# Optimization experiments

Hardware: AMD Instinct MI355X
Metric: run time of the kernel (lower is better)

The kernel has to match this reference:

```python
import jax, jax.numpy as jnp
import numpy as np

N, T, D, H1, H2, NH = 4096, 2048, 256, 128, 32, 4
ALPHA = 0.2  # LeakyReLU slope in GAT
NEG = -9e15  # mask value for non-edges


def _gat(x, adj, W, a_src, a_dst, fc_W, fc_b):
    # Multi-head GAT (pygat style), heads stacked on leading axis, then Linear fc.
    Wh = jnp.einsum('nd,hde->hne', x, W)                    # [NH, n, d_out]
    f = jnp.einsum('hne,he->hn', Wh, a_src)                 # a^T [Wh_i || .]
    g = jnp.einsum('hne,he->hn', Wh, a_dst)                 # a^T [. || Wh_j]
    e = jax.nn.leaky_relu(f[:, :, None] + g[:, None, :], ALPHA)  # [NH, n, n]
    e = jnp.where(adj[None, :, :] > 0, e, NEG)
    att = jax.nn.softmax(e, axis=-1)
    h = jax.nn.elu(jnp.einsum('hnm,hme->hne', att, Wh))     # concat=True -> ELU
    h = jnp.transpose(h, (1, 0, 2)).reshape(x.shape[0], -1)  # [n, NH*d_out]
    return h @ fc_W + fc_b


def setup_inputs() -> dict:
    key = jax.random.key(0)
    ks = jax.random.split(key, 24)
    s = 0.1
    x = jax.random.normal(ks[0], (N, D), jnp.float32)
    t_x = jax.random.normal(ks[1], (T, D), jnp.float32)
    adj = (jax.random.uniform(ks[2], (N, N)) < 0.005).astype(jnp.float32) + jnp.eye(N, dtype=jnp.float32)
    t_adj = (jax.random.uniform(ks[3], (T, T)) < 0.01).astype(jnp.float32) + jnp.eye(T, dtype=jnp.float32)
    tfidf_x = jax.random.uniform(ks[4], (T, N), jnp.float32) * 0.01
    p = lambda k, shp: jax.random.normal(k, shp, jnp.float32) * s
    return {
        'x': x, 'adj': adj, 't_x': t_x, 't_adj': t_adj, 'tfidf_x': tfidf_x,
        # concept-graph MHGAT (in D -> per-head D, concat NH*D -> fc -> D)
        'gat_W': p(ks[5], (NH, D, D)), 'gat_asrc': p(ks[6], (NH, D)), 'gat_adst': p(ks[7], (NH, D)),
        'gat_fcW': p(ks[8], (NH * D, D)), 'gat_fcb': jnp.zeros((D,), jnp.float32),
        # text-graph MHGAT
        't_W': p(ks[9], (NH, D, D)), 't_asrc': p(ks[10], (NH, D)), 't_adst': p(ks[11], (NH, D)),
        't_fcW': p(ks[12], (NH * D, D)), 't_fcb': jnp.zeros((D,), jnp.float32),
        # gated fusion fc
        'fus_W': p(ks[13], (D, D)), 'fus_b': jnp.zeros((D,), jnp.float32),
        # GCN encoder weights (Kipf VGAE GraphConvolution: adj @ (x @ W))
        'gc1_W': p(ks[14], (D, H1)), 'gc2_W': p(ks[15], (H1, H2)), 'gc3_W': p(ks[16], (H1, H2)),
    }


def reference(x, adj, t_x, t_adj, tfidf_x,
              gat_W, gat_asrc, gat_adst, gat_fcW, gat_fcb,
              t_W, t_asrc, t_adst, t_fcW, t_fcb,
              fus_W, fus_b, gc1_W, gc2_W, gc3_W):
    # gated fusion of concept-graph and text-graph GAT outputs (eval mode, dropout off)
    concept = _gat(x, adj, gat_W, gat_asrc, gat_adst, gat_fcW, gat_fcb)      # [N, D]
    gat_text = _gat(t_x, t_adj, t_W, t_asrc, t_adst, t_fcW, t_fcb)           # [T, D]
    c_text = tfidf_x.T @ gat_text                                            # [N, D]
    z = jax.nn.sigmoid(concept + c_text)
    fusion = (z * concept + (1.0 - z) * c_text) @ fus_W + fus_b              # [N, D]
    # GCN VAE encoder
    h1 = jax.nn.relu(adj @ (fusion @ gc1_W))                                 # [N, H1]
    mu = adj @ (h1 @ gc2_W)                                                  # [N, H2]
    logvar = adj @ (h1 @ gc3_W)                                              # [N, H2]
    # eval-mode reparameterize -> z_lat = mu; decoder act is identity in GCNModelVAE
    recon = mu @ mu.T                                                        # [N, N]
    return recon, mu, logvar
```

## Files before the change

### kernel.cpp

```cpp
#include <hip/hip_runtime.h>
#include <hip/hip_bf16.h>

#define MAX_E 128
typedef __attribute__((ext_vector_type(8))) short bf16x8;
typedef __attribute__((ext_vector_type(4))) float f32x4;

__device__ __forceinline__ unsigned short f2bf(float f) {
    union { float f; unsigned u; } a; a.f = f;
    unsigned r = a.u + 0x7FFFu + ((a.u >> 16) & 1u);
    return (unsigned short)(r >> 16);
}
__device__ __forceinline__ float bf2f(unsigned short s) {
    union { unsigned u; float f; } a; a.u = ((unsigned)s) << 16; return a.f;
}
__device__ __forceinline__ float wave_sum(float v) {
#pragma unroll
    for (int o = 1; o < 64; o <<= 1) v += __shfl_xor(v, o, 64);
    return v;
}
__device__ __forceinline__ float wave_max(float v) {
#pragma unroll
    for (int o = 1; o < 64; o <<= 1) v = fmaxf(v, __shfl_xor(v, o, 64));
    return v;
}

#define MAXJ 16
struct TJobs {
    const float* src[MAXJ];
    unsigned short* dst[MAXJ];
    int R[MAXJ], C[MAXJ], tb[MAXJ];
    int njobs;
};

__global__ __launch_bounds__(256) void prep_k(
        const float* __restrict__ adj, const float* __restrict__ t_adj,
        int* __restrict__ cnt, int* __restrict__ eidx_c, int* __restrict__ eidx_t,
        const float* __restrict__ gat_W, const float* __restrict__ gat_asrc,
        const float* __restrict__ gat_adst, const float* __restrict__ t_W,
        const float* __restrict__ t_asrc, const float* __restrict__ t_adst,
        float* __restrict__ APDP,
        const float* __restrict__ fus_W, const float* __restrict__ fus_b,
        const float* __restrict__ gc1_W, unsigned short* __restrict__ W2T,
        float* __restrict__ B2, int w2_base, TJobs tj) {
    __shared__ float smem[2080];
    int bid = blockIdx.x, tid = threadIdx.x;
    if (bid < 6144) {
        int* s_cnt = (int*)smem;
        if (tid == 0) *s_cnt = 0;
        __syncthreads();
        if (bid < 4096) {
            const float4* ar = (const float4*)(adj + (size_t)bid * 4096);
            int* er = eidx_c + (size_t)bid * MAX_E;
            float4 v0 = ar[tid], v1 = ar[tid + 256], v2 = ar[tid + 512], v3 = ar[tid + 768];
            float va[16] = {v0.x, v0.y, v0.z, v0.w, v1.x, v1.y, v1.z, v1.w,
                            v2.x, v2.y, v2.z, v2.w, v3.x, v3.y, v3.z, v3.w};
#pragma unroll
            for (int it = 0; it < 4; it++) {
                int jb = (tid + it * 256) * 4;
#pragma unroll
                for (int c = 0; c < 4; c++) {
                    float vv = va[it * 4 + c];
                    if (vv > 0.f) {
                        int p = atomicAdd(s_cnt, 1);
                        if (p < MAX_E) er[p] = (jb + c) | (vv > 1.5f ? 0x40000000 : 0);
                    }
                }
            }
        } else {
            int r = bid - 4096;
            const float4* ar = (const float4*)(t_adj + (size_t)r * 2048);
            int* er = eidx_t + (size_t)r * MAX_E;
            float4 v0 = ar[tid], v1 = ar[tid + 256];
            float va[8] = {v0.x, v0.y, v0.z, v0.w, v1.x, v1.y, v1.z, v1.w};
#pragma unroll
            for (int it = 0; it < 2; it++) {
                int jb = (tid + it * 256) * 4;
#pragma unroll
                for (int c = 0; c < 4; c++) {
                    if (va[it * 4 + c] > 0.f) {
                        int p = atomicAdd(s_cnt, 1);
                        if (p < MAX_E) er[p] = jb + c;
                    }
                }
            }
        }
        __syncthreads();
        if (tid == 0) cnt[bid] = *s_cnt < MAX_E ? *s_cnt : MAX_E;
    } else if (bid < 6152) {
        int pb = bid - 6144, h = pb & 3, g = pb >> 2, d = tid;
        const float* W  = g ? t_W : gat_W;
        const float* as = g ? t_asrc : gat_asrc;
        const float* ad = g ? t_adst : gat_adst;
        float* sa = smem; float* sd = smem + 256;
        sa[d] = as[h * 256 + d]; sd[d] = ad[h * 256 + d];
        __syncthreads();
        const float* wr = W + (size_t)h * 65536 + (size_t)d * 256;
        float ap = 0.f, dp = 0.f;
        for (int e = 0; e < 256; e++) { float w = wr[e]; ap += w * sa[e]; dp += w * sd[e]; }
        APDP[g * 1024 + h * 256 + d] = ap;
        APDP[2048 + g * 1024 + h * 256 + d] = dp;
    } else if (bid < w2_base) {
        int local = bid - 6152;
        int j = 0;
        while (j + 1 < tj.njobs && local >= tj.tb[j + 1]) j++;
        local -= tj.tb[j];
        int R = tj.R[j], C = tj.C[j];
        int xt = C >> 5;
        int tx = local % xt, ty = local / xt;
        const float* in = tj.src[j];
        unsigned short* outp = tj.dst[j];
        float (*t)[33] = (float(*)[33])smem;
        int jj = tid & 31, ii = tid >> 5;
        int r0 = ty * 32, c0 = tx * 32;
#pragma unroll
        for (int k = 0; k < 4; k++) { int rl = ii + k * 8; t[rl][jj] = in[(size_t)(r0 + rl) * C + c0 + jj]; }
        __syncthreads();
#pragma unroll
        for (int k = 0; k < 4; k++) { int cl = ii + k * 8; outp[(size_t)(c0 + cl) * R + r0 + jj] = f2bf(t[jj][cl]); }
    } else if (bid < w2_base + 32) {
        int bW = bid - w2_base;
        int n0 = (bW & 3) * 32, k0 = (bW >> 2) * 32;
        int nn = tid & 31, kb = (tid >> 5) * 4;
        float (*s_a)[65] = (float(*)[65])smem;
        float acc[4] = {0.f, 0.f, 0.f, 0.f};
        for (int ec = 0; ec < 4; ec++) {
            for (int t = tid; t < 32 * 64; t += 256) {
                int kk2 = t >> 6, ee = t & 63;
                s_a[kk2][ee] = fus_W[(size_t)(k0 + kk2) * 256 + ec * 64 + ee];
            }
            __syncthreads();
            for (int ee = 0; ee < 64; ee++) {
                float b = gc1_W[(size_t)(ec * 64 + ee) * 128 + n0 + nn];
#pragma unroll
                for (int c = 0; c < 4; c++) acc[c] += s_a[kb + c][ee] * b;
            }
            __syncthreads();
        }
#pragma unroll
        for (int c = 0; c < 4; c++)
            W2T[(size_t)(n0 + nn) * 256 + k0 + kb + c] = f2bf(acc[c]);
    } else {
        if (tid < 128) {
            float acc = 0.f;
            for (int k = 0; k < 256; k++) acc += fus_b[k] * gc1_W[(size_t)k * 128 + tid];
            B2[tid] = acc;
        }
    }
}

__global__ __launch_bounds__(256) void whfg_k(
        const float* __restrict__ x, const float* __restrict__ t_x,
        const unsigned short* __restrict__ WT, const unsigned short* __restrict__ TWT,
        unsigned short* __restrict__ WHC, unsigned short* __restrict__ WHT,
        const float* __restrict__ APDP, float* __restrict__ FC, float* __restrict__ GC,
        float* __restrict__ FT, float* __restrict__ GT) {
    __shared__ __align__(16) unsigned short As[64 * 40], Bs[64 * 40];
    int bid = blockIdx.x, tid = threadIdx.x;
    if (bid < 1536) {
        int g, xk, y, h;
        if (bid < 1024) { g = 0; xk = bid & 3; y = (bid >> 2) & 63; h = bid >> 8; }
        else { int b2 = bid - 1024; g = 1; xk = b2 & 3; y = (b2 >> 2) & 31; h = b2 >> 7; }
        const float* Af = g ? t_x : x;
        const unsigned short* Bt = (g ? TWT : WT) + h * 65536;
        unsigned short* C = (g ? WHT : WHC) + h * 256;
        int m0 = y * 64, n0 = xk * 64;
        int wave = tid >> 6, lane = tid & 63, quad = lane >> 4, r = lane & 15;
        int lrow = tid >> 2, lcol8 = (tid & 3) * 8;
        f32x4 acc[4] = {{0.f,0.f,0.f,0.f},{0.f,0.f,0.f,0.f},{0.f,0.f,0.f,0.f},{0.f,0.f,0.f,0.f}};
        for (int k0 = 0; k0 < 256; k0 += 32) {
            const float* ap = Af + (size_t)(m0 + lrow) * 256 + k0 + lcol8;
            float4 a0 = *(const float4*)ap;
            float4 a1 = *(const float4*)(ap + 4);
            ushort4 u0 = {f2bf(a0.x), f2bf(a0.y), f2bf(a0.z), f2bf(a0.w)};
            ushort4 u1 = {f2bf(a1.x), f2bf(a1.y), f2bf(a1.z), f2bf(a1.w)};
            uint4 bv = *(const uint4*)(Bt + (size_t)(n0 + lrow) * 256 + k0 + lcol8);
            *(ushort4*)(&As[lrow * 40 + lcol8]) = u0;
            *(ushort4*)(&As[lrow * 40 + lcol8 + 4]) = u1;
            *(uint4*)(&Bs[lrow * 40 + lcol8]) = bv;
            __syncthreads();
            bf16x8 af = *(const bf16x8*)(&As[(wave * 16 + r) * 40 + quad * 8]);
#pragma unroll
            for (int nj = 0; nj < 4; nj++) {
                bf16x8 bfr = *(const bf16x8*)(&Bs[(nj * 16 + r) * 40 + quad * 8]);
                acc[nj] = __builtin_amdgcn_mfma_f32_16x16x32_bf16(af, bfr, acc[nj], 0, 0, 0);
            }
            __syncthreads();
        }
#pragma unroll
        for (int nj = 0; nj < 4; nj++) {
            int n = n0 + nj * 16 + r;
#pragma unroll
            for (int reg = 0; reg < 4; reg++) {
                int m = m0 + wave * 16 + quad * 4 + reg;
                C[(size_t)m * 1024 + n] = f2bf(acc[nj][reg]);
            }
        }
    } else {
        int b = bid - 1536;
        int h = tid >> 6, lane = tid & 63;
        const float* xr; float* F; float* G; const float* AP; const float* DP; int n, i;
        if (b < 4096) { i = b; xr = x + (size_t)i * 256; F = FC; G = GC; AP = APDP; DP = APDP + 2048; n = 4096; }
        else { i = b - 4096; xr = t_x + (size_t)i * 256; F = FT; G = GT; AP = APDP + 1024; DP = APDP + 3072; n = 2048; }
        float vf = 0.f, vg = 0.f;
#pragma unroll
        for (int c = 0; c < 4; c++) {
            int d = c * 64 + lane;
            float xv = xr[d];
            vf += xv * AP[h * 256 + d];
            vg += xv * DP[h * 256 + d];
        }
        vf = wave_sum(vf); vg = wave_sum(vg);
        if (lane == 0) { F[h * n + i] = vf; G[h * n + i] = vg; }
    }
}

__global__ __launch_bounds__(256) void agg_all_k(const unsigned short* __restrict__ WHC,
        const unsigned short* __restrict__ WHT, const float* __restrict__ FC,
        const float* __restrict__ GC, const float* __restrict__ FT,
        const float* __restrict__ GT, const int* __restrict__ cnt,
        const int* __restrict__ eidx_c, const int* __restrict__ eidx_t,
        unsigned short* __restrict__ HCC, unsigned short* __restrict__ HCT) {
    int b = blockIdx.x, tid = threadIdx.x;
    int h = tid >> 6, lane = tid & 63;
    int ne = cnt[b];
    const unsigned short* WH; const float* F; const float* G; const int* ei;
    unsigned short* HC; int n, i;
    if (b < 4096) { i = b; n = 4096; WH = WHC; F = FC; G = GC; ei = eidx_c + (size_t)i * MAX_E; HC = HCC; }
    else { i = b - 4096; n = 2048; WH = WHT; F = FT; G = GT; ei = eidx_t + (size_t)i * MAX_E; HC = HCT; }
    __shared__ int s_col[MAX_E];
    __shared__ float s_w[4][MAX_E];
    for (int e = tid; e < ne; e += 256) s_col[e] = ei[e] & 0xFFFF;
    __syncthreads();
    float fi = F[h * n + i];
    float lmax = -1e30f;
    for (int e = lane; e < ne; e += 64) {
        float xv = fi + G[h * n + s_col[e]];
        xv = xv >= 0.f ? xv : 0.2f * xv;
        s_w[h][e] = xv;
        lmax = fmaxf(lmax, xv);
    }
    lmax = wave_max(lmax);
    float lsum = 0.f;
    for (int e = lane; e < ne; e += 64) {
        float w = __expf(s_w[h][e] - lmax);
        s_w[h][e] = w;
        lsum += w;
    }
    lsum = wave_sum(lsum);
    float inv = 1.f / lsum;
    float a0 = 0.f, a1 = 0.f, a2 = 0.f, a3 = 0.f;
    const unsigned short* base = WH + h * 256 + lane * 4;
    for (int e = 0; e < ne; e++) {
        float w = s_w[h][e];
        ushort4 q = *(const ushort4*)(base + (size_t)s_col[e] * 1024);
        a0 += w * bf2f(q.x); a1 += w * bf2f(q.y); a2 += w * bf2f(q.z); a3 += w * bf2f(q.w);
    }
    a0 *= inv; a1 *= inv; a2 *= inv; a3 *= inv;
    a0 = a0 > 0.f ? a0 : __expf(a0) - 1.f;
    a1 = a1 > 0.f ? a1 : __expf(a1) - 1.f;
    a2 = a2 > 0.f ? a2 : __expf(a2) - 1.f;
    a3 = a3 > 0.f ? a3 : __expf(a3) - 1.f;
    ushort4 st; st.x = f2bf(a0); st.y = f2bf(a1); st.z = f2bf(a2); st.w = f2bf(a3);
    *(ushort4*)(HC + (size_t)i * 1024 + h * 256 + lane * 4) = st;
}

__device__ __forceinline__ void mfma_core(const unsigned short* __restrict__ A,
        const unsigned short* __restrict__ Bt, int K, int m0, int n0,
        unsigned short* As, unsigned short* Bs, f32x4 acc[4]) {
    int tid = threadIdx.x;
    int wave = tid >> 6, lane = tid & 63, quad = lane >> 4, r = lane & 15;
    int lrow = tid >> 2, lcol8 = (tid & 3) * 8;
    for (int k0 = 0; k0 < K; k0 += 32) {
        uint4 av = *(const uint4*)(A + (size_t)(m0 + lrow) * K + k0 + lcol8);
        uint4 bv = *(const uint4*)(Bt + (size_t)(n0 + lrow) * K + k0 + lcol8);
        *(uint4*)(&As[lrow * 40 + lcol8]) = av;
        *(uint4*)(&Bs[lrow * 40 + lcol8]) = bv;
        __syncthreads();
        bf16x8 af = *(const bf16x8*)(&As[(wave * 16 + r) * 40 + quad * 8]);
#pragma unroll
        for (int nj = 0; nj < 4; nj++) {
            bf16x8 bfr = *(const bf16x8*)(&Bs[(nj * 16 + r) * 40 + quad * 8]);
            acc[nj] = __builtin_amdgcn_mfma_f32_16x16x32_bf16(af, bfr, acc[nj], 0, 0, 0);
        }
        __syncthreads();
    }
}

__global__ __launch_bounds__(256) void fc_both_k(const unsigned short* __restrict__ HCC,
        const unsigned short* __restrict__ HCT, const unsigned short* __restrict__ FCWT,
        const unsigned short* __restrict__ TFCWT, const float* __restrict__ fcb,
        const float* __restrict__ tfcb, float* __restrict__ CPT,
        unsigned short* __restrict__ GTT) {
    __shared__ __align__(16) unsigned short As[64 * 40], Bs[64 * 40];
    int z = blockIdx.z;
    int M = z ? 2048 : 4096;
    int m0 = blockIdx.y * 64, n0 = blockIdx.x * 64;
    if (m0 >= M) return;
    const unsigned short* A = z ? HCT : HCC;
    const unsigned short* Bt = z ? TFCWT : FCWT;
    const float* bias = z ? tfcb : fcb;
    f32x4 acc[4] = {{0.f,0.f,0.f,0.f},{0.f,0.f,0.f,0.f},{0.f,0.f,0.f,0.f},{0.f,0.f,0.f,0.f}};
    mfma_core(A, Bt, 1024, m0, n0, As, Bs, acc);
    int tid = threadIdx.x, wave = tid >> 6, lane = tid & 63, quad = lane >> 4, r = lane & 15;
#pragma unroll
    for (int nj = 0; nj < 4; nj++) {
        int n = n0 + nj * 16 + r;
        float bv = bias[n];
        if (z == 0) {
#pragma unroll
            for (int reg = 0; reg < 4; reg++) {
                int m = m0 + wave * 16 + quad * 4 + reg;
                CPT[(size_t)m * 256 + n] = acc[nj][reg] + bv;
            }
        } else {
            int mb = m0 + wave * 16 + quad * 4;
            ushort4 st;
            st.x = f2bf(acc[nj][0] + bv); st.y = f2bf(acc[nj][1] + bv);
            st.z = f2bf(acc[nj][2] + bv); st.w = f2bf(acc[nj][3] + bv);
            *(ushort4*)(GTT + (size_t)n * 2048 + mb) = st;
        }
    }
}

__global__ __launch_bounds__(256) void ctext_gate_k(
        const float* __restrict__ tfidf, const unsigned short* __restrict__ GTT,
        const float* __restrict__ CPT, unsigned short* __restrict__ FUSEIN) {
    __shared__ __align__(16) unsigned short As[64 * 40], Bs[64 * 40];
    int tid = threadIdx.x;
    int wave = tid >> 6, lane = tid & 63, quad = lane >> 4, r = lane & 15;
    int m0 = blockIdx.y * 64, n0 = blockIdx.x * 64;
    int kk = tid >> 3;
    int jj = tid & 7;
    int b  = kk >> 3, t7 = kk & 7;
    int lrow = tid >> 2, lcol8 = (tid & 3) * 8;
    int mfr = wave * 16 + r;
    int cswz = (mfr >> 3) & 3;
    f32x4 acc[4] = {{0.f,0.f,0.f,0.f},{0.f,0.f,0.f,0.f},{0.f,0.f,0.f,0.f},{0.f,0.f,0.f,0.f}};
    for (int k0 = 0; k0 < 2048; k0 += 32) {
        const float* ap = tfidf + (size_t)(k0 + kk) * 4096 + m0 + jj * 8;
        float4 a0 = *(const float4*)ap;
        float4 a1 = *(const float4*)(ap + 4);
        uint4 bv = *(const uint4*)(GTT + (size_t)(n0 + lrow) * 2048 + k0 + lcol8);
        float av[8] = {a0.x, a0.y, a0.z, a0.w, a1.x, a1.y, a1.z, a1.w};
#pragma unroll
        for (int i = 0; i < 8; i++) {
            int m = jj * 8 + i;
            As[m * 40 + ((b ^ (jj & 3)) * 8) + t7] = f2bf(av[i]);
        }
        *(uint4*)(&Bs[lrow * 40 + lcol8]) = bv;
        __syncthreads();
        bf16x8 af = *(const bf16x8*)(&As[mfr * 40 + ((quad ^ cswz) * 8)]);
#pragma unroll
        for (int nj = 0; nj < 4; nj++) {
            bf16x8 bfr = *(const bf16x8*)(&Bs[(nj * 16 + r) * 40 + quad * 8]);
            acc[nj] = __builtin_amdgcn_mfma_f32_16x16x32_bf16(af, bfr, acc[nj], 0, 0, 0);
        }
        __syncthreads();
    }
#pragma unroll
    for (int nj = 0; nj < 4; nj++) {
        int n = n0 + nj * 16 + r;
#pragma unroll
        for (int reg = 0; reg < 4; reg++) {
            int m = m0 + wave * 16 + quad * 4 + reg;
            float v = acc[nj][reg];
            float c = CPT[(size_t)m * 256 + n];
            float z = 1.f / (1.f + __expf(-(c + v)));
            FUSEIN[(size_t)m * 256 + n] = f2bf(z * c + (1.f - z) * v);
        }
    }
}

template <int EP>
__global__ __launch_bounds__(256) void gemm_ep_k(const unsigned short* __restrict__ A,
        const unsigned short* __restrict__ Bt, const float* __restrict__ bias,
        void* __restrict__ Cv, int M, int N, int K, int ldc) {
    __shared__ __align__(16) unsigned short As[64 * 40], Bs[64 * 40];
    int m0 = blockIdx.y * 64, n0 = blockIdx.x * 64;
    if (m0 >= M) return;
    f32x4 acc[4] = {{0.f,0.f,0.f,0.f},{0.f,0.f,0.f,0.f},{0.f,0.f,0.f,0.f},{0.f,0.f,0.f,0.f}};
    mfma_core(A, Bt, K, m0, n0, As, Bs, acc);
    int tid = threadIdx.x, wave = tid >> 6, lane = tid & 63, quad = lane >> 4, r = lane & 15;
#pragma unroll
    for (int nj = 0; nj < 4; nj++) {
        int n = n0 + nj * 16 + r;
        float bv = (EP == 1) ? bias[n] : 0.f;
#pragma unroll
        for (int reg = 0; reg < 4; reg++) {
            int m = m0 + wave * 16 + quad * 4 + reg;
            ((float*)Cv)[(size_t)m * ldc + n] = acc[nj][reg] + bv;
        }
    }
}

__global__ void spmm_h1_k(const int* __restrict__ cnt, const int* __restrict__ eidx,
                          const float* __restrict__ T1, unsigned short* __restrict__ H1B) {
    int i = blockIdx.x, tid = threadIdx.x;
    int ne = cnt[i];
    __shared__ int s_e[MAX_E];
    for (int e = tid; e < ne; e += 128) s_e[e] = eidx[(size_t)i * MAX_E + e];
    __syncthreads();
    float acc = 0.f;
    for (int e = 0; e < ne; e++) {
        int p = s_e[e];
        float v = (p & 0x40000000) ? 2.f : 1.f;
        acc += v * T1[(size_t)(p & 0xFFFF) * 128 + tid];
    }
    H1B[(size_t)i * 128 + tid] = f2bf(fmaxf(acc, 0.f));
}

__global__ void spmm_mu_k(const int* __restrict__ cnt, const int* __restrict__ eidx,
                          const unsigned short* __restrict__ H1B,
                          const unsigned short* __restrict__ GC23WT,
                          float* __restrict__ MU, float* __restrict__ LOGVAR,
                          unsigned short* __restrict__ MUBF) {
    int i = blockIdx.x, tid = threadIdx.x;
    int ne = cnt[i];
    __shared__ int s_e[MAX_E];
    __shared__ float s_a2[128];
    for (int e = tid; e < ne; e += 128) s_e[e] = eidx[(size_t)i * MAX_E + e];
    __syncthreads();
    float acc = 0.f;
    for (int e = 0; e < ne; e++) {
        int p = s_e[e];
        float v = (p & 0x40000000) ? 2.f : 1.f;
        acc += v * bf2f(H1B[(size_t)(p & 0xFFFF) * 128 + tid]);
    }
    s_a2[tid] = acc;
    __syncthreads();
    if (tid < 64) {
        const unsigned short* w = GC23WT + tid * 128;
        float o = 0.f;
        for (int k = 0; k < 128; k++) o += s_a2[k] * bf2f(w[k]);
        if (tid < 32) { MU[(size_t)i * 32 + tid] = o; MUBF[(size_t)i * 32 + tid] = f2bf(o); }
        else LOGVAR[(size_t)i * 32 + (tid - 32)] = o;
    }
}

extern "C" void kernel_launch(void* const* d_in, const int* in_sizes, int n_in,
                              void* d_out, int out_size, void* d_ws, size_t ws_size,
                              hipStream_t stream) {
    const float* x        = (const float*)d_in[0];
    const float* adj      = (const float*)d_in[1];
    const float* t_x      = (const float*)d_in[2];
    const float* t_adj    = (const float*)d_in[3];
    const float* tfidf    = (const float*)d_in[4];
    const float* gat_W    = (const float*)d_in[5];
    const float* gat_asrc = (const float*)d_in[6];
    const float* gat_adst = (const float*)d_in[7];
    const float* gat_fcW  = (const float*)d_in[8];
    const float* gat_fcb  = (const float*)d_in[9];
    const float* t_W      = (const float*)d_in[10];
    const float* t_asrc   = (const float*)d_in[11];
    const float* t_adst   = (const float*)d_in[12];
    const float* t_fcW    = (const float*)d_in[13];
    const float* t_fcb    = (const float*)d_in[14];
    const float* fus_W    = (const float*)d_in[15];
    const float* fus_b    = (const float*)d_in[16];
    const float* gc1_W    = (const float*)d_in[17];
    const float* gc2_W    = (const float*)d_in[18];
    const float* gc3_W    = (const float*)d_in[19];

    float* out = (float*)d_out;
    float* ws  = (float*)d_ws;

    unsigned short* WHC   = (unsigned short*)(ws + 0);
    unsigned short* HCC   = (unsigned short*)(ws + 2097152);
    unsigned short* WHT   = (unsigned short*)(ws + 4194304);
    unsigned short* HCT   = (unsigned short*)(ws + 5242880);
    float* CPT            = ws + 6291456;
    unsigned short* GTT   = (unsigned short*)(ws + 7340032);
    unsigned short* FUSEIN= (unsigned short*)(ws + 7602176);
    float* T1             = ws + 8126464;
    unsigned short* H1B   = (unsigned short*)(ws + 8650752);
    unsigned short* MUBF  = (unsigned short*)(ws + 8912896);
    float* FC             = ws + 8978432;
    float* GC             = ws + 8994816;
    float* FT             = ws + 9011200;
    float* GT             = ws + 9019392;
    float* APDP           = ws + 9027584;
    unsigned short* WT    = (unsigned short*)(ws + 9031680);
    unsigned short* TWT   = (unsigned short*)(ws + 9162752);
    unsigned short* FCWT  = (unsigned short*)(ws + 9293824);
    unsigned short* TFCWT = (unsigned short*)(ws + 9424896);
    unsigned short* W2T   = (unsigned short*)(ws + 9555968);
    float* B2             = ws + 9572352;
    unsigned short* GC23WT= (unsigned short*)(ws + 9572480);
    int* ECNT             = (int*)(ws + 9576576);
    int* EIDX_C           = (int*)(ws + 9582720);
    int* EIDX_T           = (int*)(ws + 10107008);
    float* MU     = out + (size_t)4096 * 4096;
    float* LOGVAR = MU + (size_t)4096 * 32;

    TJobs tj = {};
    int nj = 0, tb = 0;
    auto add = [&](const float* s, unsigned short* d, int R, int C) {
        tj.src[nj] = s; tj.dst[nj] = d; tj.R[nj] = R; tj.C[nj] = C; tj.tb[nj] = tb;
        tb += (R >> 5) * (C >> 5); nj++;
    };
    for (int h = 0; h < 4; h++) add(gat_W + h * 65536, WT + h * 65536, 256, 256);
    for (int h = 0; h < 4; h++) add(t_W + h * 65536, TWT + h * 65536, 256, 256);
    add(gat_fcW, FCWT, 1024, 256);
    add(t_fcW, TFCWT, 1024, 256);
    add(gc2_W, GC23WT, 128, 32);
    add(gc3_W, GC23WT + 32 * 128, 128, 32);
    tj.njobs = nj;
    int w2_base = 6152 + tb;
    prep_k<<<w2_base + 33, 256, 0, stream>>>(adj, t_adj, ECNT, EIDX_C, EIDX_T,
        gat_W, gat_asrc, gat_adst, t_W, t_asrc, t_adst, APDP,
        fus_W, fus_b, gc1_W, W2T, B2, w2_base, tj);

    whfg_k<<<1536 + 6144, 256, 0, stream>>>(x, t_x, WT, TWT, WHC, WHT, APDP, FC, GC, FT, GT);

    agg_all_k<<<6144, 256, 0, stream>>>(WHC, WHT, FC, GC, FT, GT, ECNT, EIDX_C, EIDX_T, HCC, HCT);

    fc_both_k<<<dim3(4, 64, 2), 256, 0, stream>>>(HCC, HCT, FCWT, TFCWT, gat_fcb, t_fcb, CPT, GTT);

    ctext_gate_k<<<dim3(4, 64), 256, 0, stream>>>(tfidf, GTT, CPT, FUSEIN);

    gemm_ep_k<1><<<dim3(2, 64), 256, 0, stream>>>(FUSEIN, W2T, B2, T1, 4096, 128, 256, 128);

    spmm_h1_k<<<4096, 128, 0, stream>>>(ECNT, EIDX_C, T1, H1B);

    spmm_mu_k<<<4096, 128, 0, stream>>>(ECNT, EIDX_C, H1B, GC23WT, MU, LOGVAR, MUBF);

    gemm_ep_k<0><<<dim3(64, 64), 256, 0, stream>>>(MUBF, MUBF, nullptr, out, 4096, 4096, 32, 4096);
}
```

Measured before the change: 356.2 us.

## Split-K the tfidf^T GEMM with separate gate kernel; pre-cast x to bf16

```diff
diff --git a/kernel.cpp b/kernel.cpp
--- a/kernel.cpp
+++ b/kernel.cpp
@@ -41,7 +41,10 @@
         float* __restrict__ APDP,
         const float* __restrict__ fus_W, const float* __restrict__ fus_b,
         const float* __restrict__ gc1_W, unsigned short* __restrict__ W2T,
-        float* __restrict__ B2, int w2_base, TJobs tj) {
+        float* __restrict__ B2,
+        const float* __restrict__ x, const float* __restrict__ t_x,
+        unsigned short* __restrict__ XBF, unsigned short* __restrict__ TXBF,
+        int w2_base, int cast_base, TJobs tj) {
     __shared__ float smem[2080];
     int bid = blockIdx.x, tid = threadIdx.x;
     if (bid < 6144) {
@@ -139,17 +142,48 @@
 #pragma unroll
         for (int c = 0; c < 4; c++)
             W2T[(size_t)(n0 + nn) * 256 + k0 + kb + c] = f2bf(acc[c]);
-    } else {
+    } else if (bid < cast_base) {
         if (tid < 128) {
             float acc = 0.f;
             for (int k = 0; k < 256; k++) acc += fus_b[k] * gc1_W[(size_t)k * 128 + tid];
             B2[tid] = acc;
         }
+    } else {
+        int local = bid - cast_base;
+        const float4* src; unsigned short* dst; int li;
+        if (local < 1024) { src = (const float4*)x; dst = XBF; li = local * 256 + tid; }
+        else { src = (const float4*)t_x; dst = TXBF; li = (local - 1024) * 256 + tid; }
+        float4 v = src[li];
+        ushort4 o = {f2bf(v.x), f2bf(v.y), f2bf(v.z), f2bf(v.w)};
+        *(ushort4*)(dst + (size_t)li * 4) = o;
+    }
+}
+
+__device__ __forceinline__ void mfma_core(const unsigned short* __restrict__ A,
+        const unsigned short* __restrict__ Bt, int K, int m0, int n0,
+        unsigned short* As, unsigned short* Bs, f32x4 acc[4]) {
+    int tid = threadIdx.x;
+    int wave = tid >> 6, lane = tid & 63, quad = lane >> 4, r = lane & 15;
+    int lrow = tid >> 2, lcol8 = (tid & 3) * 8;
+    for (int k0 = 0; k0 < K; k0 += 32) {
+        uint4 av = *(const uint4*)(A + (size_t)(m0 + lrow) * K + k0 + lcol8);
+        uint4 bv = *(const uint4*)(Bt + (size_t)(n0 + lrow) * K + k0 + lcol8);
+        *(uint4*)(&As[lrow * 40 + lcol8]) = av;
+        *(uint4*)(&Bs[lrow * 40 + lcol8]) = bv;
+        __syncthreads();
+        bf16x8 af = *(const bf16x8*)(&As[(wave * 16 + r) * 40 + quad * 8]);
+#pragma unroll
+        for (int nj = 0; nj < 4; nj++) {
+            bf16x8 bfr = *(const bf16x8*)(&Bs[(nj * 16 + r) * 40 + quad * 8]);
+            acc[nj] = __builtin_amdgcn_mfma_f32_16x16x32_bf16(af, bfr, acc[nj], 0, 0, 0);
+        }
+        __syncthreads();
     }
 }
 
 __global__ __launch_bounds__(256) void whfg_k(
         const float* __restrict__ x, const float* __restrict__ t_x,
+        const unsigned short* __restrict__ XBF, const unsigned short* __restrict__ TXBF,
         const unsigned short* __restrict__ WT, const unsigned short* __restrict__ TWT,
         unsigned short* __restrict__ WHC, unsigned short* __restrict__ WHT,
         const float* __restrict__ APDP, float* __restrict__ FC, float* __restrict__ GC,
@@ -160,32 +194,13 @@
         int g, xk, y, h;
         if (bid < 1024) { g = 0; xk = bid & 3; y = (bid >> 2) & 63; h = bid >> 8; }
         else { int b2 = bid - 1024; g = 1; xk = b2 & 3; y = (b2 >> 2) & 31; h = b2 >> 7; }
-        const float* Af = g ? t_x : x;
+        const unsigned short* A = g ? TXBF : XBF;
         const unsigned short* Bt = (g ? TWT : WT) + h * 65536;
         unsigned short* C = (g ? WHT : WHC) + h * 256;
         int m0 = y * 64, n0 = xk * 64;
+        f32x4 acc[4] = {{0.f,0.f,0.f,0.f},{0.f,0.f,0.f,0.f},{0.f,0.f,0.f,0.f},{0.f,0.f,0.f,0.f}};
+        mfma_core(A, Bt, 256, m0, n0, As, Bs, acc);
         int wave = tid >> 6, lane = tid & 63, quad = lane >> 4, r = lane & 15;
-        int lrow = tid >> 2, lcol8 = (tid & 3) * 8;
-        f32x4 acc[4] = {{0.f,0.f,0.f,0.f},{0.f,0.f,0.f,0.f},{0.f,0.f,0.f,0.f},{0.f,0.f,0.f,0.f}};
-        for (int k0 = 0; k0 < 256; k0 += 32) {
-            const float* ap = Af + (size_t)(m0 + lrow) * 256 + k0 + lcol8;
-            float4 a0 = *(const float4*)ap;
-            float4 a1 = *(const float4*)(ap + 4);
-            ushort4 u0 = {f2bf(a0.x), f2bf(a0.y), f2bf(a0.z), f2bf(a0.w)};
-            ushort4 u1 = {f2bf(a1.x), f2bf(a1.y), f2bf(a1.z), f2bf(a1.w)};
-            uint4 bv = *(const uint4*)(Bt + (size_t)(n0 + lrow) * 256 + k0 + lcol8);
-            *(ushort4*)(&As[lrow * 40 + lcol8]) = u0;
-            *(ushort4*)(&As[lrow * 40 + lcol8 + 4]) = u1;
-            *(uint4*)(&Bs[lrow * 40 + lcol8]) = bv;
-            __syncthreads();
-            bf16x8 af = *(const bf16x8*)(&As[(wave * 16 + r) * 40 + quad * 8]);
-#pragma unroll
-            for (int nj = 0; nj < 4; nj++) {
-                bf16x8 bfr = *(const bf16x8*)(&Bs[(nj * 16 + r) * 40 + quad * 8]);
-                acc[nj] = __builtin_amdgcn_mfma_f32_16x16x32_bf16(af, bfr, acc[nj], 0, 0, 0);
-            }
-            __syncthreads();
-        }
 #pragma unroll
         for (int nj = 0; nj < 4; nj++) {
             int n = n0 + nj * 16 + r;
@@ -264,28 +279,6 @@
     *(ushort4*)(HC + (size_t)i * 1024 + h * 256 + lane * 4) = st;
 }
 
-__device__ __forceinline__ void mfma_core(const unsigned short* __restrict__ A,
-        const unsigned short* __restrict__ Bt, int K, int m0, int n0,
-        unsigned short* As, unsigned short* Bs, f32x4 acc[4]) {
-    int tid = threadIdx.x;
-    int wave = tid >> 6, lane = tid & 63, quad = lane >> 4, r = lane & 15;
-    int lrow = tid >> 2, lcol8 = (tid & 3) * 8;
-    for (int k0 = 0; k0 < K; k0 += 32) {
-        uint4 av = *(const uint4*)(A + (size_t)(m0 + lrow) * K + k0 + lcol8);
-        uint4 bv = *(const uint4*)(Bt + (size_t)(n0 + lrow) * K + k0 + lcol8);
-        *(uint4*)(&As[lrow * 40 + lcol8]) = av;
-        *(uint4*)(&Bs[lrow * 40 + lcol8]) = bv;
-        __syncthreads();
-        bf16x8 af = *(const bf16x8*)(&As[(wave * 16 + r) * 40 + quad * 8]);
-#pragma unroll
-        for (int nj = 0; nj < 4; nj++) {
-            bf16x8 bfr = *(const bf16x8*)(&Bs[(nj * 16 + r) * 40 + quad * 8]);
-            acc[nj] = __builtin_amdgcn_mfma_f32_16x16x32_bf16(af, bfr, acc[nj], 0, 0, 0);
-        }
-        __syncthreads();
-    }
-}
-
 __global__ __launch_bounds__(256) void fc_both_k(const unsigned short* __restrict__ HCC,
         const unsigned short* __restrict__ HCT, const unsigned short* __restrict__ FCWT,
         const unsigned short* __restrict__ TFCWT, const float* __restrict__ fcb,
@@ -322,53 +315,71 @@
     }
 }
 
-__global__ __launch_bounds__(256) void ctext_gate_k(
+__global__ __launch_bounds__(256) void ctext_splitk_k(
         const float* __restrict__ tfidf, const unsigned short* __restrict__ GTT,
-        const float* __restrict__ CPT, unsigned short* __restrict__ FUSEIN) {
-    __shared__ __align__(16) unsigned short As[64 * 40], Bs[64 * 40];
+        float* __restrict__ PART) {
+    __shared__ float Asf[32 * 65];
     int tid = threadIdx.x;
     int wave = tid >> 6, lane = tid & 63, quad = lane >> 4, r = lane & 15;
-    int m0 = blockIdx.y * 64, n0 = blockIdx.x * 64;
-    int kk = tid >> 3;
-    int jj = tid & 7;
-    int b  = kk >> 3, t7 = kk & 7;
-    int lrow = tid >> 2, lcol8 = (tid & 3) * 8;
-    int mfr = wave * 16 + r;
-    int cswz = (mfr >> 3) & 3;
-    f32x4 acc[4] = {{0.f,0.f,0.f,0.f},{0.f,0.f,0.f,0.f},{0.f,0.f,0.f,0.f},{0.f,0.f,0.f,0.f}};
-    for (int k0 = 0; k0 < 2048; k0 += 32) {
-        const float* ap = tfidf + (size_t)(k0 + kk) * 4096 + m0 + jj * 8;
+    int kc = blockIdx.x;
+    int m0 = blockIdx.y * 64;
+    int kbase = kc * 256;
+    int akk = tid >> 3, aseg = tid & 7;
+    int mrel = wave * 16 + r;
+    f32x4 acc[16];
+#pragma unroll
+    for (int i = 0; i < 16; i++) acc[i] = {0.f, 0.f, 0.f, 0.f};
+    for (int k0 = 0; k0 < 256; k0 += 32) {
+        const float* ap = tfidf + (size_t)(kbase + k0 + akk) * 4096 + m0 + aseg * 8;
         float4 a0 = *(const float4*)ap;
         float4 a1 = *(const float4*)(ap + 4);
-        uint4 bv = *(const uint4*)(GTT + (size_t)(n0 + lrow) * 2048 + k0 + lcol8);
         float av[8] = {a0.x, a0.y, a0.z, a0.w, a1.x, a1.y, a1.z, a1.w};
-#pragma unroll
-        for (int i = 0; i < 8; i++) {
-            int m = jj * 8 + i;
-            As[m * 40 + ((b ^ (jj & 3)) * 8) + t7] = f2bf(av[i]);
-        }
-        *(uint4*)(&Bs[lrow * 40 + lcol8]) = bv;
-        __syncthreads();
-        bf16x8 af = *(const bf16x8*)(&As[mfr * 40 + ((quad ^ cswz) * 8)]);
-#pragma unroll
-        for (int nj = 0; nj < 4; nj++) {
-            bf16x8 bfr = *(const bf16x8*)(&Bs[(nj * 16 + r) * 40 + quad * 8]);
+        __syncthreads();
+#pragma unroll
+        for (int i = 0; i < 8; i++) Asf[akk * 65 + aseg * 8 + i] = av[i];
+        __syncthreads();
+        bf16x8 af;
+#pragma unroll
+        for (int j = 0; j < 8; j++)
+            af[j] = (short)f2bf(Asf[(quad * 8 + j) * 65 + mrel]);
+#pragma unroll
+        for (int nj = 0; nj < 16; nj++) {
+            bf16x8 bfr = *(const bf16x8*)(GTT + (size_t)(nj * 16 + r) * 2048
+                                          + kbase + k0 + quad * 8);
             acc[nj] = __builtin_amdgcn_mfma_f32_16x16x32_bf16(af, bfr, acc[nj], 0, 0, 0);
         }
-        __syncthreads();
-    }
-#pragma unroll
-    for (int nj = 0; nj < 4; nj++) {
-        int n = n0 + nj * 16 + r;
+    }
+    float* P = PART + (size_t)kc * (4096 * 256);
+#pragma unroll
+    for (int nj = 0; nj < 16; nj++) {
+        int n = nj * 16 + r;
 #pragma unroll
         for (int reg = 0; reg < 4; reg++) {
             int m = m0 + wave * 16 + quad * 4 + reg;
-            float v = acc[nj][reg];
-            float c = CPT[(size_t)m * 256 + n];
-            float z = 1.f / (1.f + __expf(-(c + v)));
-            FUSEIN[(size_t)m * 256 + n] = f2bf(z * c + (1.f - z) * v);
-        }
-    }
+            P[(size_t)m * 256 + n] = acc[nj][reg];
+        }
+    }
+}
+
+__global__ void gate_k(const float* __restrict__ PART, const float* __restrict__ CPT,
+                       unsigned short* __restrict__ FUSEIN) {
+    int idx = blockIdx.x * 256 + threadIdx.x;
+    float4 s = ((const float4*)PART)[idx];
+#pragma unroll
+    for (int kc = 1; kc < 8; kc++) {
+        float4 p = ((const float4*)PART)[(size_t)kc * 262144 + idx];
+        s.x += p.x; s.y += p.y; s.z += p.z; s.w += p.w;
+    }
+    float4 c = ((const float4*)CPT)[idx];
+    float cc[4] = {c.x, c.y, c.z, c.w}, ss[4] = {s.x, s.y, s.z, s.w};
+    ushort4 st;
+    unsigned short* o = (unsigned short*)&st;
+#pragma unroll
+    for (int i = 0; i < 4; i++) {
+        float z = 1.f / (1.f + __expf(-(cc[i] + ss[i])));
+        o[i] = f2bf(z * cc[i] + (1.f - z) * ss[i]);
+    }
+    *(ushort4*)(FUSEIN + (size_t)idx * 4) = st;
 }
 
 template <int EP>
@@ -468,27 +479,30 @@
     unsigned short* HCC   = (unsigned short*)(ws + 2097152);
     unsigned short* WHT   = (unsigned short*)(ws + 4194304);
     unsigned short* HCT   = (unsigned short*)(ws + 5242880);
-    float* CPT            = ws + 6291456;
-    unsigned short* GTT   = (unsigned short*)(ws + 7340032);
-    unsigned short* FUSEIN= (unsigned short*)(ws + 7602176);
-    float* T1             = ws + 8126464;
-    unsigned short* H1B   = (unsigned short*)(ws + 8650752);
-    unsigned short* MUBF  = (unsigned short*)(ws + 8912896);
-    float* FC             = ws + 8978432;
-    float* GC             = ws + 8994816;
-    float* FT             = ws + 9011200;
-    float* GT             = ws + 9019392;
-    float* APDP           = ws + 9027584;
-    unsigned short* WT    = (unsigned short*)(ws + 9031680);
-    unsigned short* TWT   = (unsigned short*)(ws + 9162752);
-    unsigned short* FCWT  = (unsigned short*)(ws + 9293824);
-    unsigned short* TFCWT = (unsigned short*)(ws + 9424896);
-    unsigned short* W2T   = (unsigned short*)(ws + 9555968);
-    float* B2             = ws + 9572352;
-    unsigned short* GC23WT= (unsigned short*)(ws + 9572480);
-    int* ECNT             = (int*)(ws + 9576576);
-    int* EIDX_C           = (int*)(ws + 9582720);
-    int* EIDX_T           = (int*)(ws + 10107008);
+    float* PART           = ws + 0;
+    float* CPT            = ws + 8388608;
+    unsigned short* GTT   = (unsigned short*)(ws + 9437184);
+    unsigned short* FUSEIN= (unsigned short*)(ws + 9699328);
+    float* T1             = ws + 10223616;
+    unsigned short* H1B   = (unsigned short*)(ws + 10747904);
+    unsigned short* MUBF  = (unsigned short*)(ws + 11010048);
+    float* FC             = ws + 11075584;
+    float* GC             = ws + 11091968;
+    float* FT             = ws + 11108352;
+    float* GT             = ws + 11116544;
+    float* APDP           = ws + 11124736;
+    unsigned short* WT    = (unsigned short*)(ws + 11128832);
+    unsigned short* TWT   = (unsigned short*)(ws + 11259904);
+    unsigned short* FCWT  = (unsigned short*)(ws + 11390976);
+    unsigned short* TFCWT = (unsigned short*)(ws + 11522048);
+    unsigned short* W2T   = (unsigned short*)(ws + 11653120);
+    float* B2             = ws + 11669504;
+    unsigned short* GC23WT= (unsigned short*)(ws + 11669632);
+    int* ECNT             = (int*)(ws + 11673728);
+    int* EIDX_C           = (int*)(ws + 11679872);
+    int* EIDX_T           = (int*)(ws + 12204160);
+    unsigned short* XBF   = (unsigned short*)(ws + 12466304);
+    unsigned short* TXBF  = (unsigned short*)(ws + 12990592);
     float* MU     = out + (size_t)4096 * 4096;
     float* LOGVAR = MU + (size_t)4096 * 32;
 
@@ -506,17 +520,21 @@
     add(gc3_W, GC23WT + 32 * 128, 128, 32);
     tj.njobs = nj;
     int w2_base = 6152 + tb;
-    prep_k<<<w2_base + 33, 256, 0, stream>>>(adj, t_adj, ECNT, EIDX_C, EIDX_T,
+    int cast_base = w2_base + 33;
+    prep_k<<<cast_base + 1536, 256, 0, stream>>>(adj, t_adj, ECNT, EIDX_C, EIDX_T,
         gat_W, gat_asrc, gat_adst, t_W, t_asrc, t_adst, APDP,
-        fus_W, fus_b, gc1_W, W2T, B2, w2_base, tj);
-
-    whfg_k<<<1536 + 6144, 256, 0, stream>>>(x, t_x, WT, TWT, WHC, WHT, APDP, FC, GC, FT, GT);
+        fus_W, fus_b, gc1_W, W2T, B2, x, t_x, XBF, TXBF, w2_base, cast_base, tj);
+
+    whfg_k<<<1536 + 6144, 256, 0, stream>>>(x, t_x, XBF, TXBF, WT, TWT, WHC, WHT,
+                                            APDP, FC, GC, FT, GT);
 
     agg_all_k<<<6144, 256, 0, stream>>>(WHC, WHT, FC, GC, FT, GT, ECNT, EIDX_C, EIDX_T, HCC, HCT);
 
     fc_both_k<<<dim3(4, 64, 2), 256, 0, stream>>>(HCC, HCT, FCWT, TFCWT, gat_fcb, t_fcb, CPT, GTT);
 
-    ctext_gate_k<<<dim3(4, 64), 256, 0, stream>>>(tfidf, GTT, CPT, FUSEIN);
+    ctext_splitk_k<<<dim3(8, 64), 256, 0, stream>>>(tfidf, GTT, PART);
+
+    gate_k<<<1024, 256, 0, stream>>>(PART, CPT, FUSEIN);
 
     gemm_ep_k<1><<<dim3(2, 64), 256, 0, stream>>>(FUSEIN, W2T, B2, T1, 4096, 128, 256, 128);
 
```

Result: faster. 346.8 us (-2.6%).
